# Optimization experiments

Hardware: AMD Instinct MI355X
Metric: run time of the kernel (lower is better)

Reference implementation:

```python
import jax, jax.numpy as jnp
import numpy as np

NUM_HEADS = 16
EPS = 1e-12  # F.normalize default eps


def _l2norm(x):
    # F.normalize(x, dim=-1): x / max(||x||_2, eps)
    n = jnp.sqrt(jnp.sum(x * x, axis=-1, keepdims=True))
    return x / jnp.maximum(n, EPS)


def setup_inputs() -> dict:
    key = jax.random.key(0)
    k1, k2, k3 = jax.random.split(key, 3)
    B, N, C = 16, 3136, 768
    x = jax.random.normal(k1, (B, N, C), dtype=jnp.float32)
    qkv_w = jax.random.normal(k2, (C, 3 * C), dtype=jnp.float32) * (1.0 / np.sqrt(C))
    temperature = jnp.ones((NUM_HEADS, 1, 1), dtype=jnp.float32)
    proj_w = jax.random.normal(k3, (C, C), dtype=jnp.float32) * (1.0 / np.sqrt(C))
    proj_b = jnp.zeros((C,), dtype=jnp.float32)
    return {"x": x, "qkv_w": qkv_w, "temperature": temperature,
            "proj_w": proj_w, "proj_b": proj_b}


def reference(x, qkv_w, temperature, proj_w, proj_b):
    B, N, C = x.shape
    H = NUM_HEADS
    D = C // H
    # qkv: [B,N,3C] -> [B,N,3,H,D] -> (3,B,H,D,N)
    qkv = (x @ qkv_w).reshape(B, N, 3, H, D).transpose(2, 0, 3, 4, 1)
    q, k, v = qkv[0], qkv[1], qkv[2]  # each [B,H,D,N]
    qn = _l2norm(q)  # normalize over token axis N
    kn = _l2norm(k)
    # cross-covariance: [B,H,D,D]
    attn = jnp.einsum('bhdn,bhen->bhde', qn, kn) * temperature
    attn = jax.nn.softmax(attn, axis=-1)
    out = jnp.einsum('bhde,bhen->bhdn', attn, v)  # [B,H,D,N]
    out = out.transpose(0, 3, 1, 2).reshape(B, N, C)
    return out @ proj_w + proj_b
```

## Files before the change

kernel.cpp:

```cpp
#include <hip/hip_runtime.h>

typedef unsigned short u16;
typedef unsigned int   u32;
typedef __attribute__((ext_vector_type(4))) float f32x4;
typedef __attribute__((ext_vector_type(8))) short bf16x8;
typedef __attribute__((ext_vector_type(8))) unsigned short u16x8;

#define MFMA16(a,b,c) __builtin_amdgcn_mfma_f32_16x16x32_bf16(a,b,c,0,0,0)

#define PANEL 2408448u

__device__ __forceinline__ u16 f32_bf16(float f){
  u32 u = __builtin_bit_cast(u32, f);
  u = (u + 0x7FFFu + ((u >> 16) & 1u)) >> 16;
  return (u16)u;
}

__device__ __forceinline__ void async_cp16(const u16* g, u16* l){
  __builtin_amdgcn_global_load_lds((const __attribute__((address_space(1))) u32*)g,
                                   (__attribute__((address_space(3))) u32*)l, 16, 0, 0);
}

__global__ __launch_bounds__(256)
void cvt_f32_bf16(const float* __restrict__ in, u16* __restrict__ out){
  size_t i = ((size_t)blockIdx.x * 256 + threadIdx.x) * 8;
  f32x4 a = *(const f32x4*)(in + i);
  f32x4 b = *(const f32x4*)(in + i + 4);
  u16x8 o;
  o[0]=f32_bf16(a[0]); o[1]=f32_bf16(a[1]); o[2]=f32_bf16(a[2]); o[3]=f32_bf16(a[3]);
  o[4]=f32_bf16(b[0]); o[5]=f32_bf16(b[1]); o[6]=f32_bf16(b[2]); o[7]=f32_bf16(b[3]);
  *(u16x8*)(out + i) = o;
}

__global__ __launch_bounds__(256)
void transpose_cvt(const float* __restrict__ w, u16* __restrict__ wt, int K, int N){
  __shared__ float tile[32][33];
  int n0 = blockIdx.x * 32, k0 = blockIdx.y * 32;
  int tx = threadIdx.x, ty = threadIdx.y;
#pragma unroll
  for (int j = 0; j < 32; j += 8) tile[ty + j][tx] = w[(size_t)(k0 + ty + j) * N + n0 + tx];
  __syncthreads();
#pragma unroll
  for (int j = 0; j < 32; j += 8)
    wt[(size_t)(n0 + ty + j) * K + k0 + tx] = f32_bf16(tile[tx][ty + j]);
}

template<int A_GATHER>
__device__ __forceinline__ void stage_half(const u16* __restrict__ G, u16* __restrict__ lds,
                                           int tid, int row0, int base, int kt, int ld){
#pragma unroll
  for (int i = 0; i < 2; i++){
    int c = i * 512 + tid;
    int r = c >> 3;
    int kc = (c & 7) ^ (r & 7);
    const u16* src;
    if (A_GATHER){
      unsigned k0 = (unsigned)(kt + kc * 8);
      unsigned hh = k0 / 48u, dd = k0 - hh * 48u;
      src = G + (size_t)hh * PANEL + (size_t)(base + row0 + r) * 48 + dd;
    } else {
      src = G + (size_t)(base + row0 + r) * ld + kt + kc * 8;
    }
    async_cp16(src, lds + ((size_t)(row0 + r) * 64 + (c & 7) * 8));
  }
}

template<int OUT_BF16, int BIAS, int A_GATHER, int C_HEADS>
__global__ __launch_bounds__(512, 2)
void gemm256(const u16* __restrict__ A, const u16* __restrict__ Bt,
             void* __restrict__ Cv, const float* __restrict__ bias,
             int K, int lda, int ldc, int nbx){
  __shared__ u16 sA[2][256 * 64];
  __shared__ u16 sB[2][256 * 64];
  const int tid  = threadIdx.x;
  const int lane = tid & 63, wave = tid >> 6;
  const int lrow = lane & 15, quad = lane >> 4;
  const int wr = wave >> 2, wc = wave & 3;

  const int nwg = (int)gridDim.x;
  const int bid = (int)blockIdx.x;
  const int qq = nwg >> 3, rm = nwg & 7;
  const int xcd = bid & 7, jj = bid >> 3;
  const int f = (xcd < rm ? xcd * (qq + 1) : rm * (qq + 1) + (xcd - rm) * qq) + jj;
  const int bx = f % nbx, by = f / nbx;
  const int m0 = by * 256, n0 = bx * 256;

  const int sw = lrow & 7;
  const int colK0 = (quad ^ sw) * 8;
  const int colK1 = ((4 + quad) ^ sw) * 8;

  f32x4 acc[8][4];
#pragma unroll
  for (int i = 0; i < 8; i++)
#pragma unroll
    for (int j = 0; j < 4; j++) acc[i][j] = (f32x4){0.f, 0.f, 0.f, 0.f};

  const int nt = K >> 6;
  stage_half<A_GATHER>(A, sA[0], tid, 0,   m0, 0, lda);
  stage_half<A_GATHER>(A, sA[0], tid, 128, m0, 0, lda);
  stage_half<0>(Bt, sB[0], tid, 0,   n0, 0, K);
  stage_half<0>(Bt, sB[0], tid, 128, n0, 0, K);
  stage_half<A_GATHER>(A, sA[1], tid, 0,   m0, 64, lda);
  stage_half<A_GATHER>(A, sA[1], tid, 128, m0, 64, lda);
  asm volatile("s_waitcnt vmcnt(4)" ::: "memory");
  __builtin_amdgcn_s_barrier();

#pragma unroll 1
  for (int t = 0; t < nt; ++t){
    u16* sAb = sA[t & 1];
    u16* sBb = sB[t & 1];
    u16* sBn = sB[(t & 1) ^ 1];
    const int kt1 = (t + 1) << 6, kt2 = (t + 2) << 6;
    bf16x8 A0[8], A1[8], B0[4], B1[4];

#pragma unroll
    for (int mi = 0; mi < 8; mi++)
      A0[mi] = *(const bf16x8*)&sAb[(wr * 128 + mi * 16 + lrow) * 64 + colK0];
#pragma unroll
    for (int ni = 0; ni < 4; ni++)
      B0[ni] = *(const bf16x8*)&sBb[(wc * 64 + ni * 16 + lrow) * 64 + colK0];
    if (t + 1 < nt) stage_half<0>(Bt, sBn, tid, 0, n0, kt1, K);
    __builtin_amdgcn_s_barrier();
    asm volatile("s_waitcnt lgkmcnt(0)" ::: "memory");
    __builtin_amdgcn_s_setprio(1);
#pragma unroll
    for (int mi = 0; mi < 8; mi++){
      acc[mi][0] = MFMA16(A0[mi], B0[0], acc[mi][0]);
      acc[mi][1] = MFMA16(A0[mi], B0[1], acc[mi][1]);
    }
    __builtin_amdgcn_s_setprio(0);
    __builtin_amdgcn_s_barrier();

#pragma unroll
    for (int mi = 0; mi < 8; mi++)
      A1[mi] = *(const bf16x8*)&sAb[(wr * 128 + mi * 16 + lrow) * 64 + colK1];
#pragma unroll
    for (int ni = 0; ni < 4; ni++)
      B1[ni] = *(const bf16x8*)&sBb[(wc * 64 + ni * 16 + lrow) * 64 + colK1];
    if (t + 1 < nt) stage_half<0>(Bt, sBn, tid, 128, n0, kt1, K);
    __builtin_amdgcn_s_barrier();
    asm volatile("s_waitcnt lgkmcnt(0)" ::: "memory");
    __builtin_amdgcn_s_setprio(1);
#pragma unroll
    for (int mi = 0; mi < 8; mi++){
      acc[mi][2] = MFMA16(A0[mi], B0[2], acc[mi][2]);
      acc[mi][3] = MFMA16(A0[mi], B0[3], acc[mi][3]);
    }
    __builtin_amdgcn_s_setprio(0);
    __builtin_amdgcn_s_barrier();

    if (t + 2 < nt) stage_half<A_GATHER>(A, sAb, tid, 0, m0, kt2, lda);
    __builtin_amdgcn_s_barrier();
    __builtin_amdgcn_s_setprio(1);
#pragma unroll
    for (int mi = 0; mi < 8; mi++){
      acc[mi][0] = MFMA16(A1[mi], B1[0], acc[mi][0]);
      acc[mi][1] = MFMA16(A1[mi], B1[1], acc[mi][1]);
    }
    __builtin_amdgcn_s_setprio(0);
    __builtin_amdgcn_s_barrier();

    if (t + 2 < nt) stage_half<A_GATHER>(A, sAb, tid, 128, m0, kt2, lda);
    __builtin_amdgcn_s_barrier();
    __builtin_amdgcn_s_setprio(1);
#pragma unroll
    for (int mi = 0; mi < 8; mi++){
      acc[mi][2] = MFMA16(A1[mi], B1[2], acc[mi][2]);
      acc[mi][3] = MFMA16(A1[mi], B1[3], acc[mi][3]);
    }
    __builtin_amdgcn_s_setprio(0);
    if (t + 2 < nt)      asm volatile("s_waitcnt vmcnt(4)" ::: "memory");
    else if (t + 1 < nt) asm volatile("s_waitcnt vmcnt(0)" ::: "memory");
    __builtin_amdgcn_s_barrier();
  }

#pragma unroll
  for (int mi = 0; mi < 8; mi++){
#pragma unroll
    for (int ni = 0; ni < 4; ni++){
      const int col = n0 + wc * 64 + ni * 16 + lrow;
      if (OUT_BF16 && C_HEADS){
        unsigned which = (unsigned)col / 768u;
        unsigned rem   = (unsigned)col - which * 768u;
        unsigned hh    = rem / 48u;
        unsigned dd    = rem - hh * 48u;
        u16* cb = (u16*)Cv + (size_t)(which * 16u + hh) * PANEL + dd;
#pragma unroll
        for (int r = 0; r < 4; r++){
          int row = m0 + wr * 128 + mi * 16 + quad * 4 + r;
          cb[(size_t)row * 48] = f32_bf16(acc[mi][ni][r]);
        }
      } else {
        float bv = BIAS ? bias[col] : 0.f;
#pragma unroll
        for (int r = 0; r < 4; r++){
          int row = m0 + wr * 128 + mi * 16 + quad * 4 + r;
          float v = acc[mi][ni][r];
          if (OUT_BF16) ((u16*)Cv)[(size_t)row * ldc + col] = f32_bf16(v);
          else          ((float*)Cv)[(size_t)row * ldc + col] = v + bv;
        }
      }
    }
  }
}

__global__ __launch_bounds__(256)
void attn_stats(const u16* __restrict__ qkv2, const float* __restrict__ temperature,
                u16* __restrict__ attnb){
  const int h = blockIdx.x, b = blockIdx.y;
  const int tid = threadIdx.x, wave = tid >> 6, lane = tid & 63;
  const int lrow = lane & 15, quad = lane >> 4;
  __shared__ struct {
    union {
      struct { u16 q[48 * 136]; u16 k[48 * 136]; } t;
      float red[2 * 15 * 256];
    } u;
    float S[48 * 49];
    float invq[48], invk[48];
  } sm;

  f32x4 acc[15];
#pragma unroll
  for (int t = 0; t < 15; t++) acc[t] = (f32x4){0.f, 0.f, 0.f, 0.f};

  const u16* qbase = qkv2 + (size_t)h        * PANEL + (size_t)b * 3136 * 48;
  const u16* kbase = qkv2 + (size_t)(16 + h) * PANEL + (size_t)b * 3136 * 48;

  for (int n0 = 0; n0 < 3136; n0 += 128){
    __syncthreads();
#pragma unroll
    for (int i = 0; i < 3; i++){
      int wgrp = i * 4 + wave;
      int qk = wgrp >= 6;
      int dg = qk ? wgrp - 6 : wgrp;
      int n  = n0 + lane * 2;
      const u16* src = (qk ? kbase : qbase) + (size_t)n * 48 + dg * 8;
      u16x8 va = (n     < 3136) ? *(const u16x8*)src        : (u16x8){0,0,0,0,0,0,0,0};
      u16x8 vb = (n + 1 < 3136) ? *(const u16x8*)(src + 48) : (u16x8){0,0,0,0,0,0,0,0};
      u16* dst = qk ? sm.u.t.k : sm.u.t.q;
#pragma unroll
      for (int j = 0; j < 8; j++)
        *(u32*)&dst[(dg * 8 + j) * 136 + lane * 2] = (u32)va[j] | ((u32)vb[j] << 16);
    }
    __syncthreads();
    bf16x8 qf[3], kf[3];
#pragma unroll
    for (int ti = 0; ti < 3; ti++){
      qf[ti] = *(const bf16x8*)&sm.u.t.q[(ti * 16 + lrow) * 136 + wave * 32 + quad * 8];
      kf[ti] = *(const bf16x8*)&sm.u.t.k[(ti * 16 + lrow) * 136 + wave * 32 + quad * 8];
    }
#pragma unroll
    for (int ti = 0; ti < 3; ti++)
#pragma unroll
      for (int tj = 0; tj < 3; tj++)
        acc[ti * 3 + tj] = MFMA16(qf[ti], kf[tj], acc[ti * 3 + tj]);
#pragma unroll
    for (int ti = 0; ti < 3; ti++){
      acc[9  + ti] = MFMA16(qf[ti], qf[ti], acc[9  + ti]);
      acc[12 + ti] = MFMA16(kf[ti], kf[ti], acc[12 + ti]);
    }
  }
  __syncthreads();
  if (wave < 2){
#pragma unroll
    for (int t = 0; t < 15; t++)
      *(f32x4*)&sm.u.red[(wave * 15 + t) * 256 + lane * 4] = acc[t];
  }
  __syncthreads();
  if (wave >= 2){
#pragma unroll
    for (int t = 0; t < 15; t++){
      f32x4* p = (f32x4*)&sm.u.red[((wave - 2) * 15 + t) * 256 + lane * 4];
      *p = *p + acc[t];
    }
  }
  __syncthreads();
  {
    const int p = tid;
    const int lr = p >> 2, r = p & 3;
    const int row16 = ((lr >> 4) << 2) + r, col16 = lr & 15;
#pragma unroll
    for (int t = 0; t < 9; t++){
      float v = sm.u.red[t * 256 + p] + sm.u.red[(15 + t) * 256 + p];
      sm.S[((t / 3) * 16 + row16) * 49 + (t % 3) * 16 + col16] = v;
    }
#pragma unroll
    for (int t = 9; t < 15; t++){
      float v = sm.u.red[t * 256 + p] + sm.u.red[(15 + t) * 256 + p];
      if (row16 == col16){
        if (t < 12) sm.invq[(t - 9)  * 16 + row16] = v;
        else        sm.invk[(t - 12) * 16 + row16] = v;
      }
    }
  }
  __syncthreads();
  if (tid < 96){
    float* arr = (tid < 48) ? sm.invq : sm.invk;
    int d = (tid < 48) ? tid : tid - 48;
    arr[d] = 1.0f / fmaxf(sqrtf(arr[d]), 1e-12f);
  }
  __syncthreads();
  if (tid < 48){
    const int d = tid;
    const float scale = sm.invq[d] * temperature[h];
    float lg[48];
    float mx = -1e30f;
#pragma unroll
    for (int e = 0; e < 48; e++){
      lg[e] = sm.S[d * 49 + e] * scale * sm.invk[e];
      mx = fmaxf(mx, lg[e]);
    }
    float s = 0.f;
#pragma unroll
    for (int e = 0; e < 48; e++){ float ex = __expf(lg[e] - mx); lg[e] = ex; s += ex; }
    const float inv = 1.f / s;
    u16* dst = attnb + ((size_t)(b * 16 + h) * 48 + d) * 64;
#pragma unroll
    for (int e = 0; e < 48; e++) dst[e] = f32_bf16(lg[e] * inv);
#pragma unroll
    for (int e = 48; e < 64; e++) dst[e] = 0;
  }
}

__global__ __launch_bounds__(256)
void attn_apply_v(const u16* __restrict__ qkv2, const u16* __restrict__ attnb,
                  u16* __restrict__ outm){
  const int h = blockIdx.y, b = blockIdx.z;
  const int nb = blockIdx.x * 256;
  const int tid = threadIdx.x, wave = tid >> 6, lane = tid & 63;
  const int lrow = lane & 15, quad = lane >> 4;
  __shared__ u16 sA[48 * 72];
#pragma unroll
  for (int i = 0; i < 2; i++){
    int idx = i * 256 + tid;
    if (idx < 384){
      int d = idx >> 3, eg = idx & 7;
      *(u16x8*)&sA[d * 72 + eg * 8] =
        *(const u16x8*)&attnb[((size_t)(b * 16 + h) * 48 + d) * 64 + eg * 8];
    }
  }
  __syncthreads();
  bf16x8 bfr[3][2];
#pragma unroll
  for (int tj = 0; tj < 3; tj++){
    bfr[tj][0] = *(const bf16x8*)&sA[(tj * 16 + lrow) * 72 + quad * 8];
    bfr[tj][1] = *(const bf16x8*)&sA[(tj * 16 + lrow) * 72 + 32 + quad * 8];
  }
  f32x4 acc[4][3];
#pragma unroll
  for (int i = 0; i < 4; i++)
#pragma unroll
    for (int j = 0; j < 3; j++) acc[i][j] = (f32x4){0.f, 0.f, 0.f, 0.f};

  const u16* vpanel = qkv2 + (size_t)(32 + h) * PANEL + (size_t)b * 3136 * 48;
  const int eo1 = 32 + ((quad < 2) ? quad * 8 : 0);
#pragma unroll
  for (int mi = 0; mi < 4; mi++){
    int n = nb + wave * 64 + mi * 16 + lrow;
    int nc = n < 3136 ? n : 3135;
    const u16* vp = vpanel + (size_t)nc * 48;
    bf16x8 a0 = *(const bf16x8*)(vp + quad * 8);
    bf16x8 a1 = *(const bf16x8*)(vp + eo1);
#pragma unroll
    for (int tj = 0; tj < 3; tj++){
      acc[mi][tj] = MFMA16(a0, bfr[tj][0], acc[mi][tj]);
      acc[mi][tj] = MFMA16(a1, bfr[tj][1], acc[mi][tj]);
    }
  }
  u16* opanel = outm + (size_t)h * PANEL + (size_t)b * 3136 * 48;
#pragma unroll
  for (int mi = 0; mi < 4; mi++)
#pragma unroll
    for (int tj = 0; tj < 3; tj++){
      int d = tj * 16 + lrow;
#pragma unroll
      for (int r = 0; r < 4; r++){
        int n = nb + wave * 64 + mi * 16 + quad * 4 + r;
        if (n < 3136) opanel[(size_t)n * 48 + d] = f32_bf16(acc[mi][tj][r]);
      }
    }
}

extern "C" void kernel_launch(void* const* d_in, const int* in_sizes, int n_in,
                              void* d_out, int out_size, void* d_ws, size_t ws_size,
                              hipStream_t stream){
  const float* x      = (const float*)d_in[0];
  const float* qkv_w  = (const float*)d_in[1];
  const float* temp   = (const float*)d_in[2];
  const float* proj_w = (const float*)d_in[3];
  const float* proj_b = (const float*)d_in[4];
  float* out = (float*)d_out;
  char* ws = (char*)d_ws;

  const size_t OFF_XB   = 0;
  const size_t OFF_WQ   = 77070336;
  const size_t OFF_WP   = 80609280;
  const size_t OFF_QKV  = 81788928;
  const size_t OFF_ATTN = 312999936;

  u16* xb    = (u16*)(ws + OFF_XB);
  u16* wqt   = (u16*)(ws + OFF_WQ);
  u16* wpt   = (u16*)(ws + OFF_WP);
  u16* qkv2  = (u16*)(ws + OFF_QKV);
  u16* attnb = (u16*)(ws + OFF_ATTN);

  cvt_f32_bf16<<<dim3(18816), dim3(256), 0, stream>>>(x, xb);
  transpose_cvt<<<dim3(2304 / 32, 768 / 32), dim3(32, 8), 0, stream>>>(qkv_w, wqt, 768, 2304);
  transpose_cvt<<<dim3(768 / 32, 768 / 32), dim3(32, 8), 0, stream>>>(proj_w, wpt, 768, 768);
  gemm256<1, 0, 0, 1><<<dim3(1764), dim3(512), 0, stream>>>(xb, wqt, qkv2, nullptr, 768, 768, 0, 9);
  attn_stats<<<dim3(16, 16), dim3(256), 0, stream>>>(qkv2, temp, attnb);
  attn_apply_v<<<dim3(13, 16, 16), dim3(256), 0, stream>>>(qkv2, attnb, qkv2);
  gemm256<0, 1, 1, 0><<<dim3(588), dim3(512), 0, stream>>>(qkv2, wpt, out, proj_b, 768, 0, 768, 3);
}
```

Before: 664.3 us.

## Reschedule GEMM main loop with interleaved wave tiling and A/B prefetch

Restructures the 256x256 bf16 GEMM main loop. Each wave now owns interleaved 16-row and 16-column strips instead of contiguous 128x64 blocks, and both K-halves of a fragment are loaded together. The double-buffer staging order is changed so that both A and B for the next tile are prefetched earlier (vmcnt 6). The aim is to spread LDS reads across four compute phases, cut fragment register pressure, and hide global latency better. The epilogue row and column mapping is updated to match, at the cost of more complex vmcnt accounting.

```diff
diff --git a/kernel.cpp b/kernel.cpp
--- a/kernel.cpp
+++ b/kernel.cpp
@@ -97,80 +97,103 @@
 
   const int nt = K >> 6;
   stage_half<A_GATHER>(A, sA[0], tid, 0,   m0, 0, lda);
-  stage_half<A_GATHER>(A, sA[0], tid, 128, m0, 0, lda);
   stage_half<0>(Bt, sB[0], tid, 0,   n0, 0, K);
   stage_half<0>(Bt, sB[0], tid, 128, n0, 0, K);
-  stage_half<A_GATHER>(A, sA[1], tid, 0,   m0, 64, lda);
-  stage_half<A_GATHER>(A, sA[1], tid, 128, m0, 64, lda);
-  asm volatile("s_waitcnt vmcnt(4)" ::: "memory");
+  stage_half<A_GATHER>(A, sA[0], tid, 128, m0, 0, lda);
+  if (nt > 1){
+    stage_half<A_GATHER>(A, sA[1], tid, 0,   m0, 64, lda);
+    stage_half<0>(Bt, sB[1], tid, 0,   n0, 64, K);
+    stage_half<0>(Bt, sB[1], tid, 128, n0, 64, K);
+    asm volatile("s_waitcnt vmcnt(6)" ::: "memory");
+  } else {
+    asm volatile("s_waitcnt vmcnt(0)" ::: "memory");
+  }
   __builtin_amdgcn_s_barrier();
 
 #pragma unroll 1
   for (int t = 0; t < nt; ++t){
-    u16* sAb = sA[t & 1];
-    u16* sBb = sB[t & 1];
-    u16* sBn = sB[(t & 1) ^ 1];
+    const int p = t & 1;
+    u16* sAb = sA[p];
+    u16* sBb = sB[p];
+    u16* sAn = sA[p ^ 1];
     const int kt1 = (t + 1) << 6, kt2 = (t + 2) << 6;
-    bf16x8 A0[8], A1[8], B0[4], B1[4];
-
-#pragma unroll
-    for (int mi = 0; mi < 8; mi++)
-      A0[mi] = *(const bf16x8*)&sAb[(wr * 128 + mi * 16 + lrow) * 64 + colK0];
-#pragma unroll
-    for (int ni = 0; ni < 4; ni++)
-      B0[ni] = *(const bf16x8*)&sBb[(wc * 64 + ni * 16 + lrow) * 64 + colK0];
-    if (t + 1 < nt) stage_half<0>(Bt, sBn, tid, 0, n0, kt1, K);
+    bf16x8 ah[4][2], bl[2][2], bh[2][2];
+
+    if (t + 1 < nt) stage_half<A_GATHER>(A, sAn, tid, 128, m0, kt1, lda);
+#pragma unroll
+    for (int mi = 0; mi < 4; mi++){
+      ah[mi][0] = *(const bf16x8*)&sAb[(mi * 32 + wr * 16 + lrow) * 64 + colK0];
+      ah[mi][1] = *(const bf16x8*)&sAb[(mi * 32 + wr * 16 + lrow) * 64 + colK1];
+    }
+#pragma unroll
+    for (int ni = 0; ni < 2; ni++){
+      bl[ni][0] = *(const bf16x8*)&sBb[(ni * 64 + wc * 16 + lrow) * 64 + colK0];
+      bl[ni][1] = *(const bf16x8*)&sBb[(ni * 64 + wc * 16 + lrow) * 64 + colK1];
+    }
     __builtin_amdgcn_s_barrier();
     asm volatile("s_waitcnt lgkmcnt(0)" ::: "memory");
     __builtin_amdgcn_s_setprio(1);
 #pragma unroll
-    for (int mi = 0; mi < 8; mi++){
-      acc[mi][0] = MFMA16(A0[mi], B0[0], acc[mi][0]);
-      acc[mi][1] = MFMA16(A0[mi], B0[1], acc[mi][1]);
-    }
+    for (int mi = 0; mi < 4; mi++)
+#pragma unroll
+      for (int ni = 0; ni < 2; ni++){
+        acc[mi][ni] = MFMA16(ah[mi][0], bl[ni][0], acc[mi][ni]);
+        acc[mi][ni] = MFMA16(ah[mi][1], bl[ni][1], acc[mi][ni]);
+      }
     __builtin_amdgcn_s_setprio(0);
     __builtin_amdgcn_s_barrier();
 
-#pragma unroll
-    for (int mi = 0; mi < 8; mi++)
-      A1[mi] = *(const bf16x8*)&sAb[(wr * 128 + mi * 16 + lrow) * 64 + colK1];
-#pragma unroll
-    for (int ni = 0; ni < 4; ni++)
-      B1[ni] = *(const bf16x8*)&sBb[(wc * 64 + ni * 16 + lrow) * 64 + colK1];
-    if (t + 1 < nt) stage_half<0>(Bt, sBn, tid, 128, n0, kt1, K);
+    if (t + 2 < nt) stage_half<A_GATHER>(A, sAb, tid, 0, m0, kt2, lda);
+#pragma unroll
+    for (int ni = 0; ni < 2; ni++){
+      bh[ni][0] = *(const bf16x8*)&sBb[((ni + 2) * 64 + wc * 16 + lrow) * 64 + colK0];
+      bh[ni][1] = *(const bf16x8*)&sBb[((ni + 2) * 64 + wc * 16 + lrow) * 64 + colK1];
+    }
     __builtin_amdgcn_s_barrier();
     asm volatile("s_waitcnt lgkmcnt(0)" ::: "memory");
     __builtin_amdgcn_s_setprio(1);
 #pragma unroll
-    for (int mi = 0; mi < 8; mi++){
-      acc[mi][2] = MFMA16(A0[mi], B0[2], acc[mi][2]);
-      acc[mi][3] = MFMA16(A0[mi], B0[3], acc[mi][3]);
-    }
+    for (int mi = 0; mi < 4; mi++)
+#pragma unroll
+      for (int ni = 0; ni < 2; ni++){
+        acc[mi][ni + 2] = MFMA16(ah[mi][0], bh[ni][0], acc[mi][ni + 2]);
+        acc[mi][ni + 2] = MFMA16(ah[mi][1], bh[ni][1], acc[mi][ni + 2]);
+      }
     __builtin_amdgcn_s_setprio(0);
     __builtin_amdgcn_s_barrier();
 
-    if (t + 2 < nt) stage_half<A_GATHER>(A, sAb, tid, 0, m0, kt2, lda);
-    __builtin_amdgcn_s_barrier();
+    if (t + 2 < nt) stage_half<0>(Bt, sBb, tid, 0, n0, kt2, K);
+#pragma unroll
+    for (int mi = 0; mi < 4; mi++){
+      ah[mi][0] = *(const bf16x8*)&sAb[((mi + 4) * 32 + wr * 16 + lrow) * 64 + colK0];
+      ah[mi][1] = *(const bf16x8*)&sAb[((mi + 4) * 32 + wr * 16 + lrow) * 64 + colK1];
+    }
+    __builtin_amdgcn_s_barrier();
+    asm volatile("s_waitcnt lgkmcnt(0)" ::: "memory");
     __builtin_amdgcn_s_setprio(1);
 #pragma unroll
-    for (int mi = 0; mi < 8; mi++){
-      acc[mi][0] = MFMA16(A1[mi], B1[0], acc[mi][0]);
-      acc[mi][1] = MFMA16(A1[mi], B1[1], acc[mi][1]);
-    }
+    for (int mi = 0; mi < 4; mi++)
+#pragma unroll
+      for (int ni = 0; ni < 2; ni++){
+        acc[4 + mi][ni] = MFMA16(ah[mi][0], bl[ni][0], acc[4 + mi][ni]);
+        acc[4 + mi][ni] = MFMA16(ah[mi][1], bl[ni][1], acc[4 + mi][ni]);
+      }
     __builtin_amdgcn_s_setprio(0);
     __builtin_amdgcn_s_barrier();
 
-    if (t + 2 < nt) stage_half<A_GATHER>(A, sAb, tid, 128, m0, kt2, lda);
+    if (t + 2 < nt) stage_half<0>(Bt, sBb, tid, 128, n0, kt2, K);
     __builtin_amdgcn_s_barrier();
     __builtin_amdgcn_s_setprio(1);
 #pragma unroll
-    for (int mi = 0; mi < 8; mi++){
-      acc[mi][2] = MFMA16(A1[mi], B1[2], acc[mi][2]);
-      acc[mi][3] = MFMA16(A1[mi], B1[3], acc[mi][3]);
-    }
+    for (int mi = 0; mi < 4; mi++)
+#pragma unroll
+      for (int ni = 0; ni < 2; ni++){
+        acc[4 + mi][ni + 2] = MFMA16(ah[mi][0], bh[ni][0], acc[4 + mi][ni + 2]);
+        acc[4 + mi][ni + 2] = MFMA16(ah[mi][1], bh[ni][1], acc[4 + mi][ni + 2]);
+      }
     __builtin_amdgcn_s_setprio(0);
-    if (t + 2 < nt)      asm volatile("s_waitcnt vmcnt(4)" ::: "memory");
-    else if (t + 1 < nt) asm volatile("s_waitcnt vmcnt(0)" ::: "memory");
+    if (t < nt - 2)       asm volatile("s_waitcnt vmcnt(6)" ::: "memory");
+    else if (t == nt - 2) asm volatile("s_waitcnt vmcnt(0)" ::: "memory");
     __builtin_amdgcn_s_barrier();
   }
 
@@ -178,7 +201,7 @@
   for (int mi = 0; mi < 8; mi++){
 #pragma unroll
     for (int ni = 0; ni < 4; ni++){
-      const int col = n0 + wc * 64 + ni * 16 + lrow;
+      const int col = n0 + ni * 64 + wc * 16 + lrow;
       if (OUT_BF16 && C_HEADS){
         unsigned which = (unsigned)col / 768u;
         unsigned rem   = (unsigned)col - which * 768u;
@@ -187,14 +210,14 @@
         u16* cb = (u16*)Cv + (size_t)(which * 16u + hh) * PANEL + dd;
 #pragma unroll
         for (int r = 0; r < 4; r++){
-          int row = m0 + wr * 128 + mi * 16 + quad * 4 + r;
+          int row = m0 + mi * 32 + wr * 16 + quad * 4 + r;
           cb[(size_t)row * 48] = f32_bf16(acc[mi][ni][r]);
         }
       } else {
         float bv = BIAS ? bias[col] : 0.f;
 #pragma unroll
         for (int r = 0; r < 4; r++){
-          int row = m0 + wr * 128 + mi * 16 + quad * 4 + r;
+          int row = m0 + mi * 32 + wr * 16 + quad * 4 + r;
           float v = acc[mi][ni][r];
           if (OUT_BF16) ((u16*)Cv)[(size_t)row * ldc + col] = f32_bf16(v);
           else          ((float*)Cv)[(size_t)row * ldc + col] = v + bv;
```

New measurement: 699.0 us. 1.05x slower.

## Simplify GEMM main loop to two barriers with interleaved warp tile mapping

Applied to the files above, without the earlier changes.

Replaces the eight-barrier, four-phase ping-pong GEMM loop (with setprio MFMA clusters) by a simpler schedule: issue the next B tile loads up front, read all A/B fragments for both k-halves, run all 64 MFMAs, then stage the next A tile. Warp-to-tile mapping changes from contiguous 128-row/64-col blocks to interleaved 16-row/16-col strides, with the epilogue indexing updated to match. The aim is to cut barrier and priority-switch overhead and let the compiler schedule LDS reads and MFMAs freely. In exchange it raises register pressure by holding all fragments at once and loses the explicit overlap of LDS reads with MFMA phases.

```diff
diff --git a/kernel.cpp b/kernel.cpp
--- a/kernel.cpp
+++ b/kernel.cpp
@@ -100,85 +100,69 @@
   stage_half<A_GATHER>(A, sA[0], tid, 128, m0, 0, lda);
   stage_half<0>(Bt, sB[0], tid, 0,   n0, 0, K);
   stage_half<0>(Bt, sB[0], tid, 128, n0, 0, K);
-  stage_half<A_GATHER>(A, sA[1], tid, 0,   m0, 64, lda);
-  stage_half<A_GATHER>(A, sA[1], tid, 128, m0, 64, lda);
-  asm volatile("s_waitcnt vmcnt(4)" ::: "memory");
+  if (nt > 1){
+    stage_half<A_GATHER>(A, sA[1], tid, 0,   m0, 64, lda);
+    stage_half<A_GATHER>(A, sA[1], tid, 128, m0, 64, lda);
+    asm volatile("s_waitcnt vmcnt(4)" ::: "memory");
+  } else {
+    asm volatile("s_waitcnt vmcnt(0)" ::: "memory");
+  }
   __builtin_amdgcn_s_barrier();
 
 #pragma unroll 1
   for (int t = 0; t < nt; ++t){
-    u16* sAb = sA[t & 1];
-    u16* sBb = sB[t & 1];
-    u16* sBn = sB[(t & 1) ^ 1];
+    const int p = t & 1;
+    u16* sAb = sA[p];
+    u16* sBb = sB[p];
     const int kt1 = (t + 1) << 6, kt2 = (t + 2) << 6;
-    bf16x8 A0[8], A1[8], B0[4], B1[4];
-
+
+    if (t + 1 < nt){
+      stage_half<0>(Bt, sB[p ^ 1], tid, 0,   n0, kt1, K);
+      stage_half<0>(Bt, sB[p ^ 1], tid, 128, n0, kt1, K);
+    }
+
+    bf16x8 a0[8], a1[8], b0[4], b1[4];
 #pragma unroll
     for (int mi = 0; mi < 8; mi++)
-      A0[mi] = *(const bf16x8*)&sAb[(wr * 128 + mi * 16 + lrow) * 64 + colK0];
+      a0[mi] = *(const bf16x8*)&sAb[(mi * 32 + wr * 16 + lrow) * 64 + colK0];
 #pragma unroll
     for (int ni = 0; ni < 4; ni++)
-      B0[ni] = *(const bf16x8*)&sBb[(wc * 64 + ni * 16 + lrow) * 64 + colK0];
-    if (t + 1 < nt) stage_half<0>(Bt, sBn, tid, 0, n0, kt1, K);
+      b0[ni] = *(const bf16x8*)&sBb[(ni * 64 + wc * 16 + lrow) * 64 + colK0];
+#pragma unroll
+    for (int mi = 0; mi < 8; mi++)
+      a1[mi] = *(const bf16x8*)&sAb[(mi * 32 + wr * 16 + lrow) * 64 + colK1];
+#pragma unroll
+    for (int ni = 0; ni < 4; ni++)
+      b1[ni] = *(const bf16x8*)&sBb[(ni * 64 + wc * 16 + lrow) * 64 + colK1];
+
+#pragma unroll
+    for (int mi = 0; mi < 8; mi++)
+#pragma unroll
+      for (int ni = 0; ni < 4; ni++)
+        acc[mi][ni] = MFMA16(a0[mi], b0[ni], acc[mi][ni]);
+#pragma unroll
+    for (int mi = 0; mi < 8; mi++)
+#pragma unroll
+      for (int ni = 0; ni < 4; ni++)
+        acc[mi][ni] = MFMA16(a1[mi], b1[ni], acc[mi][ni]);
+
     __builtin_amdgcn_s_barrier();
-    asm volatile("s_waitcnt lgkmcnt(0)" ::: "memory");
-    __builtin_amdgcn_s_setprio(1);
-#pragma unroll
-    for (int mi = 0; mi < 8; mi++){
-      acc[mi][0] = MFMA16(A0[mi], B0[0], acc[mi][0]);
-      acc[mi][1] = MFMA16(A0[mi], B0[1], acc[mi][1]);
-    }
-    __builtin_amdgcn_s_setprio(0);
+
+    if (t + 2 < nt){
+      stage_half<A_GATHER>(A, sAb, tid, 0,   m0, kt2, lda);
+      stage_half<A_GATHER>(A, sAb, tid, 128, m0, kt2, lda);
+      asm volatile("s_waitcnt vmcnt(4)" ::: "memory");
+    } else if (t + 1 < nt){
+      asm volatile("s_waitcnt vmcnt(0)" ::: "memory");
+    }
     __builtin_amdgcn_s_barrier();
-
-#pragma unroll
-    for (int mi = 0; mi < 8; mi++)
-      A1[mi] = *(const bf16x8*)&sAb[(wr * 128 + mi * 16 + lrow) * 64 + colK1];
-#pragma unroll
-    for (int ni = 0; ni < 4; ni++)
-      B1[ni] = *(const bf16x8*)&sBb[(wc * 64 + ni * 16 + lrow) * 64 + colK1];
-    if (t + 1 < nt) stage_half<0>(Bt, sBn, tid, 128, n0, kt1, K);
-    __builtin_amdgcn_s_barrier();
-    asm volatile("s_waitcnt lgkmcnt(0)" ::: "memory");
-    __builtin_amdgcn_s_setprio(1);
-#pragma unroll
-    for (int mi = 0; mi < 8; mi++){
-      acc[mi][2] = MFMA16(A0[mi], B0[2], acc[mi][2]);
-      acc[mi][3] = MFMA16(A0[mi], B0[3], acc[mi][3]);
-    }
-    __builtin_amdgcn_s_setprio(0);
-    __builtin_amdgcn_s_barrier();
-
-    if (t + 2 < nt) stage_half<A_GATHER>(A, sAb, tid, 0, m0, kt2, lda);
-    __builtin_amdgcn_s_barrier();
-    __builtin_amdgcn_s_setprio(1);
-#pragma unroll
-    for (int mi = 0; mi < 8; mi++){
-      acc[mi][0] = MFMA16(A1[mi], B1[0], acc[mi][0]);
-      acc[mi][1] = MFMA16(A1[mi], B1[1], acc[mi][1]);
-    }
-    __builtin_amdgcn_s_setprio(0);
-    __builtin_amdgcn_s_barrier();
-
-    if (t + 2 < nt) stage_half<A_GATHER>(A, sAb, tid, 128, m0, kt2, lda);
-    __builtin_amdgcn_s_barrier();
-    __builtin_amdgcn_s_setprio(1);
-#pragma unroll
-    for (int mi = 0; mi < 8; mi++){
-      acc[mi][2] = MFMA16(A1[mi], B1[2], acc[mi][2]);
-      acc[mi][3] = MFMA16(A1[mi], B1[3], acc[mi][3]);
-    }
-    __builtin_amdgcn_s_setprio(0);
-    if (t + 2 < nt)      asm volatile("s_waitcnt vmcnt(4)" ::: "memory");
-    else if (t + 1 < nt) asm volatile("s_waitcnt vmcnt(0)" ::: "memory");
-    __builtin_amdgcn_s_barrier();
   }
 
 #pragma unroll
   for (int mi = 0; mi < 8; mi++){
 #pragma unroll
     for (int ni = 0; ni < 4; ni++){
-      const int col = n0 + wc * 64 + ni * 16 + lrow;
+      const int col = n0 + ni * 64 + wc * 16 + lrow;
       if (OUT_BF16 && C_HEADS){
         unsigned which = (unsigned)col / 768u;
         unsigned rem   = (unsigned)col - which * 768u;
@@ -187,14 +171,14 @@
         u16* cb = (u16*)Cv + (size_t)(which * 16u + hh) * PANEL + dd;
 #pragma unroll
         for (int r = 0; r < 4; r++){
-          int row = m0 + wr * 128 + mi * 16 + quad * 4 + r;
+          int row = m0 + mi * 32 + wr * 16 + quad * 4 + r;
           cb[(size_t)row * 48] = f32_bf16(acc[mi][ni][r]);
         }
       } else {
         float bv = BIAS ? bias[col] : 0.f;
 #pragma unroll
         for (int r = 0; r < 4; r++){
-          int row = m0 + wr * 128 + mi * 16 + quad * 4 + r;
+          int row = m0 + mi * 32 + wr * 16 + quad * 4 + r;
           float v = acc[mi][ni][r];
           if (OUT_BF16) ((u16*)Cv)[(size_t)row * ldc + col] = f32_bf16(v);
           else          ((float*)Cv)[(size_t)row * ldc + col] = v + bv;
```

Result: slower. 690.0 us (+3.9%).
